# Performance work log

Hardware: AMD Instinct MI355X
Metric: run time of the kernel (lower is better)

The kernel has to match this reference:

```python
import jax, jax.numpy as jnp
import numpy as np

T, B, D = 2048, 8, 1024
INIT_ALPHA_BIAS = 2.0
INIT_SCALE = 0.1


def setup_inputs() -> dict:
    key = jax.random.key(0)
    k_x, k_wa, k_wv = jax.random.split(key, 3)
    # xavier_uniform bound for (D, D): sqrt(6 / (D + D))
    bound = float(np.sqrt(6.0 / (D + D)))
    x = jax.random.normal(k_x, (T, B, D), dtype=jnp.float32)
    W_alpha = jax.random.uniform(k_wa, (D, D), jnp.float32, -bound, bound)
    W_v = jax.random.uniform(k_wv, (D, D), jnp.float32, -bound, bound) * INIT_SCALE
    b_alpha = jnp.full((D,), INIT_ALPHA_BIAS, dtype=jnp.float32)
    b_v = jnp.zeros((D,), dtype=jnp.float32)
    return {"x": x, "W_alpha": W_alpha, "b_alpha": b_alpha, "W_v": W_v, "b_v": b_v}


def reference(x, W_alpha, b_alpha, W_v, b_v):
    # x: (T, B, D)
    Tn, Bn, Dn = x.shape
    h0 = jnp.zeros((Bn, Dn), dtype=x.dtype)
    # Precompute gates/inputs for all steps (two (T*B, D) x (D, D) GEMMs)
    alpha_all = jax.nn.sigmoid(jnp.einsum('tbd,ed->tbe', x, W_alpha) + b_alpha)
    v_all = jnp.einsum('tbd,ed->tbe', x, W_v) + b_v

    def step(h_prev, av):
        a, v = av
        h_new = a * h_prev + v
        return h_new, h_new

    _, hs = jax.lax.scan(step, h0, (alpha_all, v_all))  # hs: (T, B, D)
    # output_t = h_t * silu(h_t) = h_t^2 * sigmoid(h_t)
    output = hs * (hs * jax.nn.sigmoid(hs))
    h = jnp.concatenate([h0[None], hs], axis=0)  # (T+1, B, D), h0 prepended
    return output, h
```

## Files before the change

kernel.cpp:

```cpp
#include <hip/hip_runtime.h>
#include <hip/hip_bf16.h>
#include <math.h>

#define T_STEPS 2048
#define B_SZ 8
#define D_SZ 1024
#define M_SZ (T_STEPS * B_SZ)
#define K_SZ D_SZ
#define N_SZ (2 * D_SZ)

#define BM 128
#define BN 128
#define BK 32
#define LDSS 40

typedef __attribute__((ext_vector_type(8))) short bf16x8;
typedef __attribute__((ext_vector_type(4))) float f32x4;

__device__ __forceinline__ float sigmoidf_(float z) {
    return 1.0f / (1.0f + __expf(-z));
}

__device__ __forceinline__ ushort bf16_rne(float f, float* back) {
    uint u = __float_as_uint(f);
    uint r = (u + 0x7FFFu + ((u >> 16) & 1u)) >> 16;
    *back = __uint_as_float(r << 16);
    return (ushort)r;
}

__global__ __launch_bounds__(256) void gemm_gates(
    const float* __restrict__ x,
    const float* __restrict__ Wa,
    const float* __restrict__ ba,
    const float* __restrict__ Wv,
    const float* __restrict__ bv,
    float* __restrict__ out)
{
    __shared__ ushort sAh[BM * LDSS];
    __shared__ ushort sAl[BM * LDSS];
    __shared__ ushort sBh[BN * LDSS];
    __shared__ ushort sBl[BN * LDSS];

    const int m0 = blockIdx.x * BM;
    const int n0 = blockIdx.y * BN;

    const bool is_v = (n0 >= D_SZ);
    const float* W = is_v ? (Wv + (size_t)(n0 - D_SZ) * K_SZ) : (Wa + (size_t)n0 * K_SZ);

    const int tid = threadIdx.x;
    const int wid = tid >> 6;
    const int lane = tid & 63;
    const int wm = wid >> 1;
    const int wn = wid & 1;
    const int l15 = lane & 15;
    const int l4 = lane >> 4;

    const int r0 = tid >> 3;
    const int c4 = tid & 7;

    const float* xp = x + (size_t)(m0 + r0) * K_SZ + c4 * 4;
    const float* wp = W + (size_t)r0 * K_SZ + c4 * 4;

    f32x4 acc[4][4];
    #pragma unroll
    for (int i = 0; i < 4; ++i)
        #pragma unroll
        for (int j = 0; j < 4; ++j)
            acc[i][j] = (f32x4){0.f, 0.f, 0.f, 0.f};

    for (int k0 = 0; k0 < K_SZ; k0 += BK) {
        float4 areg[4], breg[4];
        #pragma unroll
        for (int p = 0; p < 4; ++p) {
            areg[p] = *reinterpret_cast<const float4*>(xp + k0 + (size_t)(32 * p) * K_SZ);
            breg[p] = *reinterpret_cast<const float4*>(wp + k0 + (size_t)(32 * p) * K_SZ);
        }

        __syncthreads();

        #pragma unroll
        for (int p = 0; p < 4; ++p) {
            const int e = (r0 + 32 * p) * LDSS + c4 * 4;
            float bk;
            ushort4 hi, lo;
            float fa[4] = {areg[p].x, areg[p].y, areg[p].z, areg[p].w};
            hi.x = bf16_rne(fa[0], &bk); lo.x = bf16_rne(fa[0] - bk, &bk);
            hi.y = bf16_rne(fa[1], &bk); lo.y = bf16_rne(fa[1] - bk, &bk);
            hi.z = bf16_rne(fa[2], &bk); lo.z = bf16_rne(fa[2] - bk, &bk);
            hi.w = bf16_rne(fa[3], &bk); lo.w = bf16_rne(fa[3] - bk, &bk);
            *reinterpret_cast<ushort4*>(&sAh[e]) = hi;
            *reinterpret_cast<ushort4*>(&sAl[e]) = lo;
            float fb[4] = {breg[p].x, breg[p].y, breg[p].z, breg[p].w};
            hi.x = bf16_rne(fb[0], &bk); lo.x = bf16_rne(fb[0] - bk, &bk);
            hi.y = bf16_rne(fb[1], &bk); lo.y = bf16_rne(fb[1] - bk, &bk);
            hi.z = bf16_rne(fb[2], &bk); lo.z = bf16_rne(fb[2] - bk, &bk);
            hi.w = bf16_rne(fb[3], &bk); lo.w = bf16_rne(fb[3] - bk, &bk);
            *reinterpret_cast<ushort4*>(&sBh[e]) = hi;
            *reinterpret_cast<ushort4*>(&sBl[e]) = lo;
        }

        __syncthreads();

        bf16x8 ah[4], al[4];
        #pragma unroll
        for (int i = 0; i < 4; ++i) {
            const int r = wm * 64 + i * 16 + l15;
            ah[i] = *reinterpret_cast<const bf16x8*>(&sAh[r * LDSS + l4 * 8]);
            al[i] = *reinterpret_cast<const bf16x8*>(&sAl[r * LDSS + l4 * 8]);
        }
        #pragma unroll
        for (int j = 0; j < 4; ++j) {
            const int c = wn * 64 + j * 16 + l15;
            const bf16x8 bh = *reinterpret_cast<const bf16x8*>(&sBh[c * LDSS + l4 * 8]);
            const bf16x8 bl = *reinterpret_cast<const bf16x8*>(&sBl[c * LDSS + l4 * 8]);
            #pragma unroll
            for (int i = 0; i < 4; ++i) {
                acc[i][j] = __builtin_amdgcn_mfma_f32_16x16x32_bf16(ah[i], bh, acc[i][j], 0, 0, 0);
                acc[i][j] = __builtin_amdgcn_mfma_f32_16x16x32_bf16(al[i], bh, acc[i][j], 0, 0, 0);
                acc[i][j] = __builtin_amdgcn_mfma_f32_16x16x32_bf16(ah[i], bl, acc[i][j], 0, 0, 0);
            }
        }
    }

    float* hbuf = out + (size_t)M_SZ * D_SZ;
    #pragma unroll
    for (int j = 0; j < 4; ++j) {
        const int n = n0 + wn * 64 + j * 16 + l15;
        const float bb = is_v ? bv[n - D_SZ] : ba[n];
        #pragma unroll
        for (int i = 0; i < 4; ++i) {
            const int mb = m0 + wm * 64 + i * 16 + l4 * 4;
            #pragma unroll
            for (int r = 0; r < 4; ++r) {
                const int m = mb + r;
                const float z = acc[i][j][r] + bb;
                if (!is_v) {
                    out[(size_t)m * D_SZ + n] = sigmoidf_(z);
                } else {
                    hbuf[(size_t)(m + B_SZ) * D_SZ + (n - D_SZ)] = z;
                }
            }
        }
    }
}

#define SC_LANES 16
#define SC_CHUNKS 64
#define SC_LEN (T_STEPS / SC_CHUNKS)

__global__ __launch_bounds__(1024) void scan_hier(float* __restrict__ out)
{
    __shared__ float sP[SC_CHUNKS][SC_LANES];
    __shared__ float sQ[SC_CHUNKS][SC_LANES];
    __shared__ float sS[SC_CHUNKS][SC_LANES];

    float* alpha = out;
    float* hbuf = out + (size_t)M_SZ * D_SZ;

    const int tid = threadIdx.x;
    const int c = tid >> 4;
    const int l = tid & 15;
    const int bd = blockIdx.x * SC_LANES + l;
    const int t0 = c * SC_LEN;
    const int STRIDE = B_SZ * D_SZ;

    float P = 1.f, q = 0.f;
    {
        size_t idx = (size_t)t0 * STRIDE + bd;
        #pragma unroll 4
        for (int s = 0; s < SC_LEN; ++s) {
            const float a = alpha[idx];
            const float v = hbuf[idx + STRIDE];
            q = fmaf(a, q, v);
            P *= a;
            idx += STRIDE;
        }
    }
    sP[c][l] = P;
    sQ[c][l] = q;
    __syncthreads();

    if (tid < SC_LANES) {
        float s = 0.f;
        #pragma unroll 8
        for (int w = 0; w < SC_CHUNKS; ++w) {
            sS[w][tid] = s;
            s = fmaf(sP[w][tid], s, sQ[w][tid]);
        }
        hbuf[blockIdx.x * SC_LANES + tid] = 0.f;
    }
    __syncthreads();

    float h = sS[c][l];
    {
        size_t idx = (size_t)t0 * STRIDE + bd;
        #pragma unroll 4
        for (int s = 0; s < SC_LEN; ++s) {
            const float a = alpha[idx];
            const float v = hbuf[idx + STRIDE];
            h = fmaf(a, h, v);
            hbuf[idx + STRIDE] = h;
            alpha[idx] = h * h * sigmoidf_(h);
            idx += STRIDE;
        }
    }
}

extern "C" void kernel_launch(void* const* d_in, const int* in_sizes, int n_in,
                              void* d_out, int out_size, void* d_ws, size_t ws_size,
                              hipStream_t stream) {
    const float* x  = (const float*)d_in[0];
    const float* Wa = (const float*)d_in[1];
    const float* ba = (const float*)d_in[2];
    const float* Wv = (const float*)d_in[3];
    const float* bv = (const float*)d_in[4];
    float* out = (float*)d_out;

    dim3 grid(M_SZ / BM, N_SZ / BN);
    gemm_gates<<<grid, 256, 0, stream>>>(x, Wa, ba, Wv, bv, out);

    scan_hier<<<(B_SZ * D_SZ) / SC_LANES, 1024, 0, stream>>>(out);
}
```

Baseline: 489.0 us.

## Pre-split inputs to bf16 hi/lo in workspace and split scan into kernels

Adds a conversion pass that splits x and both weight matrices into bf16 hi/lo arrays in the workspace once. The GEMM then loads pre-split bf16 data into an XOR-swizzled shared tile, so the per-tile float-to-bf16 conversion is no longer repeated for every N-block. The scan is also split into three kernels (partial, combine, final) using 64-thread blocks and workspace buffers. In exchange, the conversion adds an extra read and write of x, plus extra kernel launches. The old fused path is kept as a fallback when the workspace is too small.

```diff
diff --git a/kernel.cpp b/kernel.cpp
--- a/kernel.cpp
+++ b/kernel.cpp
@@ -12,7 +12,6 @@
 #define BM 128
 #define BN 128
 #define BK 32
-#define LDSS 40
 
 typedef __attribute__((ext_vector_type(8))) short bf16x8;
 typedef __attribute__((ext_vector_type(4))) float f32x4;
@@ -28,24 +27,46 @@
     return (ushort)r;
 }
 
-__global__ __launch_bounds__(256) void gemm_gates(
-    const float* __restrict__ x,
-    const float* __restrict__ Wa,
-    const float* __restrict__ ba,
-    const float* __restrict__ Wv,
-    const float* __restrict__ bv,
+__global__ __launch_bounds__(256) void conv_split(
+    const float* __restrict__ src,
+    ushort* __restrict__ dh,
+    ushort* __restrict__ dl,
+    int n8)
+{
+    const int i = blockIdx.x * 256 + threadIdx.x;
+    if (i >= n8) return;
+    const size_t base = (size_t)i * 8;
+    const float4 f0 = *reinterpret_cast<const float4*>(src + base);
+    const float4 f1 = *reinterpret_cast<const float4*>(src + base + 4);
+    const float f[8] = {f0.x, f0.y, f0.z, f0.w, f1.x, f1.y, f1.z, f1.w};
+    ushort hi[8], lo[8];
+    #pragma unroll
+    for (int j = 0; j < 8; ++j) {
+        float back;
+        hi[j] = bf16_rne(f[j], &back);
+        float dummy;
+        lo[j] = bf16_rne(f[j] - back, &dummy);
+    }
+    *reinterpret_cast<uint4*>(dh + base) = *reinterpret_cast<const uint4*>(hi);
+    *reinterpret_cast<uint4*>(dl + base) = *reinterpret_cast<const uint4*>(lo);
+}
+
+__global__ __launch_bounds__(256) void gemm_gates2(
+    const ushort* __restrict__ xh, const ushort* __restrict__ xl,
+    const ushort* __restrict__ Wah, const ushort* __restrict__ Wal,
+    const ushort* __restrict__ Wvh, const ushort* __restrict__ Wvl,
+    const float* __restrict__ ba, const float* __restrict__ bv,
     float* __restrict__ out)
 {
-    __shared__ ushort sAh[BM * LDSS];
-    __shared__ ushort sAl[BM * LDSS];
-    __shared__ ushort sBh[BN * LDSS];
-    __shared__ ushort sBl[BN * LDSS];
+    __shared__ ushort sA[BM * 64];
+    __shared__ ushort sB[BN * 64];
 
     const int m0 = blockIdx.x * BM;
     const int n0 = blockIdx.y * BN;
-
     const bool is_v = (n0 >= D_SZ);
-    const float* W = is_v ? (Wv + (size_t)(n0 - D_SZ) * K_SZ) : (Wa + (size_t)n0 * K_SZ);
+    const int n0l = is_v ? (n0 - D_SZ) : n0;
+    const ushort* Bh = (is_v ? Wvh : Wah) + (size_t)n0l * K_SZ;
+    const ushort* Bl = (is_v ? Wvl : Wal) + (size_t)n0l * K_SZ;
 
     const int tid = threadIdx.x;
     const int wid = tid >> 6;
@@ -56,10 +77,11 @@
     const int l4 = lane >> 4;
 
     const int r0 = tid >> 3;
-    const int c4 = tid & 7;
-
-    const float* xp = x + (size_t)(m0 + r0) * K_SZ + c4 * 4;
-    const float* wp = W + (size_t)r0 * K_SZ + c4 * 4;
+    const int c = tid & 7;
+    const int kc = (c & 3) * 8;
+
+    const ushort* Asrc = (c < 4) ? xh : xl;
+    const ushort* Bsrc = (c < 4) ? Bh : Bl;
 
     f32x4 acc[4][4];
     #pragma unroll
@@ -69,15 +91,183 @@
             acc[i][j] = (f32x4){0.f, 0.f, 0.f, 0.f};
 
     for (int k0 = 0; k0 < K_SZ; k0 += BK) {
+        uint4 areg[4], breg[4];
+        #pragma unroll
+        for (int p = 0; p < 4; ++p) {
+            areg[p] = *reinterpret_cast<const uint4*>(
+                Asrc + (size_t)(m0 + r0 + 32 * p) * K_SZ + k0 + kc);
+            breg[p] = *reinterpret_cast<const uint4*>(
+                Bsrc + (size_t)(r0 + 32 * p) * K_SZ + k0 + kc);
+        }
+
+        __syncthreads();
+
+        #pragma unroll
+        for (int p = 0; p < 4; ++p) {
+            const int row = r0 + 32 * p;
+            const int phys = c ^ (row & 7);
+            *reinterpret_cast<uint4*>(&sA[row * 64 + phys * 8]) = areg[p];
+            *reinterpret_cast<uint4*>(&sB[row * 64 + phys * 8]) = breg[p];
+        }
+
+        __syncthreads();
+
+        bf16x8 ah[4], al[4];
+        #pragma unroll
+        for (int i = 0; i < 4; ++i) {
+            const int r = wm * 64 + i * 16 + l15;
+            const int ph = (l4) ^ (r & 7);
+            const int pl = (4 + l4) ^ (r & 7);
+            ah[i] = *reinterpret_cast<const bf16x8*>(&sA[r * 64 + ph * 8]);
+            al[i] = *reinterpret_cast<const bf16x8*>(&sA[r * 64 + pl * 8]);
+        }
+        #pragma unroll
+        for (int j = 0; j < 4; ++j) {
+            const int cr = wn * 64 + j * 16 + l15;
+            const int ph = (l4) ^ (cr & 7);
+            const int pl = (4 + l4) ^ (cr & 7);
+            const bf16x8 bh = *reinterpret_cast<const bf16x8*>(&sB[cr * 64 + ph * 8]);
+            const bf16x8 bl = *reinterpret_cast<const bf16x8*>(&sB[cr * 64 + pl * 8]);
+            #pragma unroll
+            for (int i = 0; i < 4; ++i) {
+                acc[i][j] = __builtin_amdgcn_mfma_f32_16x16x32_bf16(ah[i], bh, acc[i][j], 0, 0, 0);
+                acc[i][j] = __builtin_amdgcn_mfma_f32_16x16x32_bf16(al[i], bh, acc[i][j], 0, 0, 0);
+                acc[i][j] = __builtin_amdgcn_mfma_f32_16x16x32_bf16(ah[i], bl, acc[i][j], 0, 0, 0);
+            }
+        }
+    }
+
+    float* hbuf = out + (size_t)M_SZ * D_SZ;
+    #pragma unroll
+    for (int j = 0; j < 4; ++j) {
+        const int n = n0 + wn * 64 + j * 16 + l15;
+        const float bb = is_v ? bv[n - D_SZ] : ba[n];
+        #pragma unroll
+        for (int i = 0; i < 4; ++i) {
+            const int mb = m0 + wm * 64 + i * 16 + l4 * 4;
+            #pragma unroll
+            for (int r = 0; r < 4; ++r) {
+                const int m = mb + r;
+                const float z = acc[i][j][r] + bb;
+                if (!is_v) {
+                    out[(size_t)m * D_SZ + n] = sigmoidf_(z);
+                } else {
+                    hbuf[(size_t)(m + B_SZ) * D_SZ + (n - D_SZ)] = z;
+                }
+            }
+        }
+    }
+}
+
+#define NCHUNK 64
+#define CLEN (T_STEPS / NCHUNK)
+#define STRIDE (B_SZ * D_SZ)
+
+__global__ __launch_bounds__(64) void scan_part(
+    const float* __restrict__ out, float* __restrict__ P, float* __restrict__ Q)
+{
+    const int bd = blockIdx.x * 64 + threadIdx.x;
+    const int chunk = blockIdx.y;
+    const float* alpha = out;
+    const float* hbuf = out + (size_t)M_SZ * D_SZ;
+
+    float Pa = 1.f, q = 0.f;
+    size_t idx = (size_t)(chunk * CLEN) * STRIDE + bd;
+    #pragma unroll 4
+    for (int s = 0; s < CLEN; ++s) {
+        const float a = alpha[idx];
+        const float v = hbuf[idx + STRIDE];
+        q = fmaf(a, q, v);
+        Pa *= a;
+        idx += STRIDE;
+    }
+    P[(size_t)chunk * STRIDE + bd] = Pa;
+    Q[(size_t)chunk * STRIDE + bd] = q;
+}
+
+__global__ __launch_bounds__(64) void scan_comb(
+    float* __restrict__ out, const float* __restrict__ P,
+    const float* __restrict__ Q, float* __restrict__ S)
+{
+    const int bd = blockIdx.x * 64 + threadIdx.x;
+    float* hbuf = out + (size_t)M_SZ * D_SZ;
+    float s = 0.f;
+    #pragma unroll 8
+    for (int c = 0; c < NCHUNK; ++c) {
+        S[(size_t)c * STRIDE + bd] = s;
+        s = fmaf(P[(size_t)c * STRIDE + bd], s, Q[(size_t)c * STRIDE + bd]);
+    }
+    hbuf[bd] = 0.f;
+}
+
+__global__ __launch_bounds__(64) void scan_final(
+    float* __restrict__ out, const float* __restrict__ S)
+{
+    const int bd = blockIdx.x * 64 + threadIdx.x;
+    const int chunk = blockIdx.y;
+    float* alpha = out;
+    float* hbuf = out + (size_t)M_SZ * D_SZ;
+
+    float h = S[(size_t)chunk * STRIDE + bd];
+    size_t idx = (size_t)(chunk * CLEN) * STRIDE + bd;
+    #pragma unroll 4
+    for (int s = 0; s < CLEN; ++s) {
+        const float a = alpha[idx];
+        const float v = hbuf[idx + STRIDE];
+        h = fmaf(a, h, v);
+        hbuf[idx + STRIDE] = h;
+        alpha[idx] = h * h * sigmoidf_(h);
+        idx += STRIDE;
+    }
+}
+
+#define LDSS 40
+__global__ __launch_bounds__(256) void gemm_gates_fb(
+    const float* __restrict__ x,
+    const float* __restrict__ Wa,
+    const float* __restrict__ ba,
+    const float* __restrict__ Wv,
+    const float* __restrict__ bv,
+    float* __restrict__ out)
+{
+    __shared__ ushort sAh[BM * LDSS];
+    __shared__ ushort sAl[BM * LDSS];
+    __shared__ ushort sBh[BN * LDSS];
+    __shared__ ushort sBl[BN * LDSS];
+
+    const int m0 = blockIdx.x * BM;
+    const int n0 = blockIdx.y * BN;
+    const bool is_v = (n0 >= D_SZ);
+    const float* W = is_v ? (Wv + (size_t)(n0 - D_SZ) * K_SZ) : (Wa + (size_t)n0 * K_SZ);
+
+    const int tid = threadIdx.x;
+    const int wid = tid >> 6;
+    const int lane = tid & 63;
+    const int wm = wid >> 1;
+    const int wn = wid & 1;
+    const int l15 = lane & 15;
+    const int l4 = lane >> 4;
+    const int r0 = tid >> 3;
+    const int c4 = tid & 7;
+
+    const float* xp = x + (size_t)(m0 + r0) * K_SZ + c4 * 4;
+    const float* wp = W + (size_t)r0 * K_SZ + c4 * 4;
+
+    f32x4 acc[4][4];
+    #pragma unroll
+    for (int i = 0; i < 4; ++i)
+        #pragma unroll
+        for (int j = 0; j < 4; ++j)
+            acc[i][j] = (f32x4){0.f, 0.f, 0.f, 0.f};
+
+    for (int k0 = 0; k0 < K_SZ; k0 += BK) {
         float4 areg[4], breg[4];
         #pragma unroll
         for (int p = 0; p < 4; ++p) {
             areg[p] = *reinterpret_cast<const float4*>(xp + k0 + (size_t)(32 * p) * K_SZ);
             breg[p] = *reinterpret_cast<const float4*>(wp + k0 + (size_t)(32 * p) * K_SZ);
         }
-
         __syncthreads();
-
         #pragma unroll
         for (int p = 0; p < 4; ++p) {
             const int e = (r0 + 32 * p) * LDSS + c4 * 4;
@@ -98,7 +288,6 @@
             *reinterpret_cast<ushort4*>(&sBh[e]) = hi;
             *reinterpret_cast<ushort4*>(&sBl[e]) = lo;
         }
-
         __syncthreads();
 
         bf16x8 ah[4], al[4];
@@ -156,13 +345,11 @@
 
     float* alpha = out;
     float* hbuf = out + (size_t)M_SZ * D_SZ;
-
     const int tid = threadIdx.x;
     const int c = tid >> 4;
     const int l = tid & 15;
     const int bd = blockIdx.x * SC_LANES + l;
     const int t0 = c * SC_LEN;
-    const int STRIDE = B_SZ * D_SZ;
 
     float P = 1.f, q = 0.f;
     {
@@ -216,8 +403,35 @@
     const float* bv = (const float*)d_in[4];
     float* out = (float*)d_out;
 
-    dim3 grid(M_SZ / BM, N_SZ / BN);
-    gemm_gates<<<grid, 256, 0, stream>>>(x, Wa, ba, Wv, bv, out);
-
-    scan_hier<<<(B_SZ * D_SZ) / SC_LANES, 1024, 0, stream>>>(out);
-}
+    const size_t MB = 1024 * 1024;
+    const size_t need = 78 * MB;
+
+    if (ws_size >= need) {
+        char* ws = (char*)d_ws;
+        ushort* xh  = (ushort*)(ws);
+        ushort* xl  = (ushort*)(ws + 32 * MB);
+        ushort* Wah = (ushort*)(ws + 64 * MB);
+        ushort* Wal = (ushort*)(ws + 66 * MB);
+        ushort* Wvh = (ushort*)(ws + 68 * MB);
+        ushort* Wvl = (ushort*)(ws + 70 * MB);
+        float* P = (float*)(ws + 72 * MB);
+        float* Q = (float*)(ws + 74 * MB);
+        float* S = (float*)(ws + 76 * MB);
+
+        conv_split<<<(M_SZ * K_SZ / 8 + 255) / 256, 256, 0, stream>>>(x, xh, xl, M_SZ * K_SZ / 8);
+        conv_split<<<(D_SZ * K_SZ / 8 + 255) / 256, 256, 0, stream>>>(Wa, Wah, Wal, D_SZ * K_SZ / 8);
+        conv_split<<<(D_SZ * K_SZ / 8 + 255) / 256, 256, 0, stream>>>(Wv, Wvh, Wvl, D_SZ * K_SZ / 8);
+
+        dim3 grid(M_SZ / BM, N_SZ / BN);
+        gemm_gates2<<<grid, 256, 0, stream>>>(xh, xl, Wah, Wal, Wvh, Wvl, ba, bv, out);
+
+        dim3 sg(B_SZ * D_SZ / 64, NCHUNK);
+        scan_part<<<sg, 64, 0, stream>>>(out, P, Q);
+        scan_comb<<<B_SZ * D_SZ / 64, 64, 0, stream>>>(out, P, Q, S);
+        scan_final<<<sg, 64, 0, stream>>>(out, S);
+    } else {
+        dim3 grid(M_SZ / BM, N_SZ / BN);
+        gemm_gates_fb<<<grid, 256, 0, stream>>>(x, Wa, ba, Wv, bv, out);
+        scan_hier<<<(B_SZ * D_SZ) / SC_LANES, 1024, 0, stream>>>(out);
+    }
+}
```

Result: slower. 882.6 us (+80.5%).
